# Optimization experiments

Hardware: AMD Instinct MI355X
Metric: run time of the kernel (lower is better)

## Reference

```python
import jax, jax.numpy as jnp
import numpy as np

B, S, D, H, FF, R, NB = 8, 1024, 768, 12, 3072, 16, 768


def _ln(x, g, b, eps=1e-6):
    m = x.mean(-1, keepdims=True)
    v = jnp.mean((x - m) ** 2, axis=-1, keepdims=True)
    return (x - m) * jax.lax.rsqrt(v + eps) * g + b


def setup_inputs() -> dict:
    key = jax.random.key(0)

    def rn(i, shape, s=0.02):
        return jax.random.normal(jax.random.fold_in(key, i), shape, jnp.float32) * s

    inp = {
        "x": jax.random.normal(jax.random.fold_in(key, 0), (B, S, D), jnp.float32),
        "attn_mask": jnp.zeros((S, S), jnp.float32),
        "norm1_g": jnp.ones((D,), jnp.float32),
        "norm1_b": jnp.zeros((D,), jnp.float32),
        "q_w": rn(1, (D, D)), "q_b": jnp.zeros((D,), jnp.float32),
        "k_w": rn(2, (D, D)), "k_b": jnp.zeros((D,), jnp.float32),
        "v_w": rn(3, (D, D)), "v_b": jnp.zeros((D,), jnp.float32),
        "o_w": rn(4, (D, D)), "o_b": jnp.zeros((D,), jnp.float32),
        "norm2_g": jnp.ones((D,), jnp.float32),
        "norm2_b": jnp.zeros((D,), jnp.float32),
        "fc1_w": rn(5, (FF, D)), "fc1_b": jnp.zeros((FF,), jnp.float32),
        "fc2_w": rn(6, (D, FF)), "fc2_b": jnp.zeros((D,), jnp.float32),
        # shared LoRA (backbone tokens)
        "lora1_A": rn(7, (D, R)), "lora1_B": rn(8, (R, FF)),
        "lora2_A": rn(9, (FF, R)), "lora2_B": rn(10, (R, D)),
        # expert VeRA: frozen shared A/B, per-expert diagonal scaling vectors
        "vera1_A": rn(11, (D, R)), "vera1_B": rn(12, (R, FF)),
        "vera2_A": rn(13, (FF, R)), "vera2_B": rn(14, (R, D)),
        "expert_fc1_d": rn(15, (R,), 1.0), "expert_fc1_b": rn(16, (FF,), 1.0),
        "expert_fc2_d": rn(17, (R,), 1.0), "expert_fc2_b": rn(18, (D,), 1.0),
        "num_backbone_tokens": NB,
    }
    return inp


def reference(x, attn_mask, norm1_g, norm1_b, q_w, q_b, k_w, k_b, v_w, v_b,
              o_w, o_b, norm2_g, norm2_b, fc1_w, fc1_b, fc2_w, fc2_b,
              lora1_A, lora1_B, lora2_A, lora2_B,
              vera1_A, vera1_B, vera2_A, vera2_B,
              expert_fc1_d, expert_fc1_b, expert_fc2_d, expert_fc2_b,
              num_backbone_tokens):
    bsz, seq, dim = x.shape
    hd = dim // H                      # head_dim = 64
    scale = hd ** -0.5
    nb = num_backbone_tokens

    # ---- attention (manual bmm + mask + softmax, eval-mode dropout = identity) ----
    h = _ln(x, norm1_g, norm1_b)
    q = (h @ q_w.T + q_b).reshape(bsz, seq, H, hd)
    k = (h @ k_w.T + k_b).reshape(bsz, seq, H, hd)
    v = (h @ v_w.T + v_b).reshape(bsz, seq, H, hd)
    scores = jnp.einsum('bqhd,bkhd->bhqk', q * scale, k) + attn_mask  # [B,H,S,S]
    probs = jax.nn.softmax(scores, axis=-1)
    ao = jnp.einsum('bhqk,bkhd->bqhd', probs, v).reshape(bsz, seq, dim)
    x = x + (ao @ o_w.T + o_b)

    # ---- MLP with split backbone (shared LoRA) / expert (VeRA) adapters ----
    residual = x
    n2 = _ln(x, norm2_g, norm2_b)
    hid = n2 @ fc1_w.T + fc1_b                                   # [B,S,FF]
    hid_b = hid[:, :nb] + (n2[:, :nb] @ lora1_A) @ lora1_B
    hid_e = hid[:, nb:] + (((n2[:, nb:] @ vera1_A) * expert_fc1_d) @ vera1_B) * expert_fc1_b
    hid = jnp.concatenate([hid_b, hid_e], axis=1)
    hid = jax.nn.gelu(hid)
    out = hid @ fc2_w.T + fc2_b                                  # [B,S,D]
    out_b = out[:, :nb] + (hid[:, :nb] @ lora2_A) @ lora2_B
    out_e = out[:, nb:] + (((hid[:, nb:] @ vera2_A) * expert_fc2_d) @ vera2_B) * expert_fc2_b
    out = jnp.concatenate([out_b, out_e], axis=1)
    return residual + out
```

## Files before the change

kernel.cpp:

```cpp
#include <hip/hip_runtime.h>
#include <stdint.h>

#define B_  8
#define S_  1024
#define D_  768
#define H_  12
#define HD_ 64
#define FF_ 3072
#define M_  (B_*S_)
#define R_  16
#define QLD 2304
#define KBLK 128

typedef unsigned short u16;
typedef short s16x8 __attribute__((ext_vector_type(8)));
typedef float fx4  __attribute__((ext_vector_type(4)));

__device__ __forceinline__ float b2f(u16 u) {
  union { unsigned int i; float f; } c; c.i = ((unsigned int)u) << 16; return c.f;
}
__device__ __forceinline__ u16 f2b(float f) {
  union { float f; unsigned int i; } c; c.f = f;
  unsigned int x = c.i;
  x += 0x7FFFu + ((x >> 16) & 1u);
  return (u16)(x >> 16);
}
__device__ __forceinline__ float gelu_f(float x) {
  float u = 0.7978845608028654f * (x + 0.044715f * x * x * x);
  float e = __expf(2.f * u);
  float t = 1.f - 2.f / (e + 1.f);
  return 0.5f * x * (1.f + t);
}
__device__ __forceinline__ void gload16(const u16* gsrc, u16* ldst) {
  __builtin_amdgcn_global_load_lds(
      (__attribute__((address_space(1))) void*)(gsrc),
      (__attribute__((address_space(3))) void*)(ldst), 16, 0, 0);
}

__global__ __launch_bounds__(256)
void cvt_all(const float* __restrict__ q_w, const float* __restrict__ k_w,
             const float* __restrict__ v_w, const float* __restrict__ o_w,
             const float* __restrict__ fc1_w, const float* __restrict__ fc2_w,
             u16* __restrict__ wqkv, u16* __restrict__ wo,
             u16* __restrict__ wfc1, u16* __restrict__ wfc2)
{
  const int i = blockIdx.x * 256 + threadIdx.x;
  const int q1  = D_ * D_ / 4;
  const int fd4 = FF_ * D_ / 4;
  const float* s; u16* d; int j;
  if      (i <     q1)       { s = q_w;   d = wqkv;            j = i; }
  else if (i < 2 * q1)       { s = k_w;   d = wqkv + D_*D_;    j = i - q1; }
  else if (i < 3 * q1)       { s = v_w;   d = wqkv + 2*D_*D_;  j = i - 2*q1; }
  else if (i < 4 * q1)       { s = o_w;   d = wo;              j = i - 3*q1; }
  else if (i < 4 * q1 + fd4) { s = fc1_w; d = wfc1;            j = i - 4*q1; }
  else                       { s = fc2_w; d = wfc2;            j = i - 4*q1 - fd4; }
  const float4 f = ((const float4*)s)[j];
  ushort4 o4; o4.x = f2b(f.x); o4.y = f2b(f.y); o4.z = f2b(f.z); o4.w = f2b(f.w);
  ((ushort4*)d)[j] = o4;
}

__global__ __launch_bounds__(256)
void prep_all(const float* __restrict__ q_bv, const float* __restrict__ k_bv,
              const float* __restrict__ v_bv, float* __restrict__ qkvb,
              const float* __restrict__ lora1B, const float* __restrict__ vera1B,
              const float* __restrict__ e1b, u16* __restrict__ up1L, u16* __restrict__ up1V,
              const float* __restrict__ lora2B, const float* __restrict__ vera2B,
              const float* __restrict__ e2b, u16* __restrict__ up2L, u16* __restrict__ up2V,
              const float* __restrict__ lora2A, const float* __restrict__ vera2A,
              u16* __restrict__ a2tL, u16* __restrict__ a2tV)
{
  const int f = blockIdx.x * 256 + threadIdx.x;
  if (f < QLD)
    qkvb[f] = (f < D_) ? q_bv[f] : (f < 2 * D_) ? k_bv[f - D_] : v_bv[f - 2 * D_];
  {
    const float ev = e1b[f];
    #pragma unroll
    for (int r = 0; r < 16; ++r) {
      up1L[(size_t)f * 32 + r] = f2b(lora1B[(size_t)r * FF_ + f]);
      up1V[(size_t)f * 32 + r] = f2b(vera1B[(size_t)r * FF_ + f] * ev);
      up1L[(size_t)f * 32 + 16 + r] = 0;
      up1V[(size_t)f * 32 + 16 + r] = 0;
    }
  }
  {
    const float4* apl = (const float4*)(lora2A + (size_t)f * 16);
    const float4* apv = (const float4*)(vera2A + (size_t)f * 16);
    #pragma unroll
    for (int q4 = 0; q4 < 4; ++q4) {
      const float4 l4 = apl[q4], v4 = apv[q4];
      a2tL[(size_t)(q4*4+0) * FF_ + f] = f2b(l4.x);
      a2tL[(size_t)(q4*4+1) * FF_ + f] = f2b(l4.y);
      a2tL[(size_t)(q4*4+2) * FF_ + f] = f2b(l4.z);
      a2tL[(size_t)(q4*4+3) * FF_ + f] = f2b(l4.w);
      a2tV[(size_t)(q4*4+0) * FF_ + f] = f2b(v4.x);
      a2tV[(size_t)(q4*4+1) * FF_ + f] = f2b(v4.y);
      a2tV[(size_t)(q4*4+2) * FF_ + f] = f2b(v4.z);
      a2tV[(size_t)(q4*4+3) * FF_ + f] = f2b(v4.w);
    }
  }
  if (f < D_) {
    const float ev = e2b[f];
    #pragma unroll
    for (int r = 0; r < 16; ++r) {
      up2L[(size_t)f * 32 + r] = f2b(lora2B[(size_t)r * D_ + f]);
      up2V[(size_t)f * 32 + r] = f2b(vera2B[(size_t)r * D_ + f] * ev);
      up2L[(size_t)f * 32 + 16 + r] = 0;
      up2V[(size_t)f * 32 + 16 + r] = 0;
    }
  }
}

template<bool ADD>
__global__ __launch_bounds__(256)
void ln_k(const float* __restrict__ x, const u16* __restrict__ add,
          const float* __restrict__ g, const float* __restrict__ beta,
          u16* __restrict__ outb, float* __restrict__ xsum,
          const float* __restrict__ Alora, const float* __restrict__ Avera,
          const float* __restrict__ dvec, u16* __restrict__ tmp1b,
          const int* __restrict__ nbp)
{
  const int row = blockIdx.x;
  const size_t base = (size_t)row * D_;
  float v0[3]; float s = 0.f, sq = 0.f;
  #pragma unroll
  for (int i = 0; i < 3; ++i) {
    const int d = threadIdx.x + i * 256;
    float val = x[base + d];
    if (ADD) { val += b2f(add[base + d]); xsum[base + d] = val; }
    v0[i] = val; s += val; sq += val * val;
  }
  #pragma unroll
  for (int mm = 32; mm >= 1; mm >>= 1) { s += __shfl_xor(s, mm); sq += __shfl_xor(sq, mm); }
  __shared__ float ss[4], s2[4];
  if ((threadIdx.x & 63) == 0) { ss[threadIdx.x >> 6] = s; s2[threadIdx.x >> 6] = sq; }
  __syncthreads();
  s  = ss[0] + ss[1] + ss[2] + ss[3];
  sq = s2[0] + s2[1] + s2[2] + s2[3];
  const float mean = s * (1.f / D_);
  const float var  = sq * (1.f / D_) - mean * mean;
  const float rs   = rsqrtf(var + 1e-6f);
  float nv[3];
  #pragma unroll
  for (int i = 0; i < 3; ++i) {
    const int d = threadIdx.x + i * 256;
    nv[i] = (v0[i] - mean) * rs * g[d] + beta[d];
    outb[base + d] = f2b(nv[i]);
  }

  if (ADD) {
    const int nb = *nbp;
    const bool ex = (row % S_) >= nb;
    const float* Am = ex ? Avera : Alora;
    float p[16];
    #pragma unroll
    for (int r = 0; r < 16; ++r) p[r] = 0.f;
    #pragma unroll
    for (int i = 0; i < 3; ++i) {
      const int d = threadIdx.x + i * 256;
      const float4* ap = (const float4*)(Am + (size_t)d * R_);
      const float4 a0 = ap[0], a1 = ap[1], a2 = ap[2], a3 = ap[3];
      const float vv = nv[i];
      p[0]  += vv * a0.x; p[1]  += vv * a0.y; p[2]  += vv * a0.z; p[3]  += vv * a0.w;
      p[4]  += vv * a1.x; p[5]  += vv * a1.y; p[6]  += vv * a1.z; p[7]  += vv * a1.w;
      p[8]  += vv * a2.x; p[9]  += vv * a2.y; p[10] += vv * a2.z; p[11] += vv * a2.w;
      p[12] += vv * a3.x; p[13] += vv * a3.y; p[14] += vv * a3.z; p[15] += vv * a3.w;
    }
    #pragma unroll
    for (int st = 1; st < 16; st <<= 1)
      #pragma unroll
      for (int r = 0; r < 16; ++r) p[r] += __shfl_xor(p[r], st);
    __shared__ float sred[16][16];
    const int grp = threadIdx.x >> 4;
    if ((threadIdx.x & 15) == 0) {
      #pragma unroll
      for (int r = 0; r < 16; ++r) sred[grp][r] = p[r];
    }
    __syncthreads();
    if (threadIdx.x < 16) {
      float v = 0.f;
      #pragma unroll
      for (int gg = 0; gg < 16; ++gg) v += sred[gg][threadIdx.x];
      if (ex) v *= dvec[threadIdx.x];
      tmp1b[(size_t)row * 32 + threadIdx.x] = f2b(v);
      tmp1b[(size_t)row * 32 + 16 + threadIdx.x] = 0;
    }
  }
}

template<int MODE>
__global__ __launch_bounds__(256)
void gemm_bt(const u16* __restrict__ A, const u16* __restrict__ W,
             const float* __restrict__ bias, u16* __restrict__ Cb,
             float* __restrict__ Cf, const float* __restrict__ resid,
             const u16* __restrict__ Aad, const u16* __restrict__ BadL,
             const u16* __restrict__ BadV, const int* __restrict__ nbp,
             int M, int N, int K)
{
  __shared__ u16 As[128 * 32];
  __shared__ u16 Bs[128 * 32];
  const int tid   = threadIdx.x;
  const int lane  = tid & 63;
  const int wid   = tid >> 6;
  const int wr    = wid >> 1;
  const int wc    = wid & 1;
  const int lr    = lane & 15;
  const int lk    = (lane >> 4) << 3;
  const int gn    = N >> 7;
  const int nwg   = (M >> 7) * gn;
  const int chunk = nwg >> 3;
  const int lin   = blockIdx.x;
  const int swz   = (lin & 7) * chunk + (lin >> 3);
  const int m0    = (swz / gn) * 128;
  const int n0    = (swz % gn) * 128;
  const int kg    = (tid & 3) * 8;
  const int row_a = tid >> 2;

  fx4 acc[4][4];
  const fx4 zero = {0.f, 0.f, 0.f, 0.f};
  #pragma unroll
  for (int i = 0; i < 4; ++i)
    #pragma unroll
    for (int j = 0; j < 4; ++j) acc[i][j] = zero;

  for (int k0 = 0; k0 < K; k0 += 32) {
    #pragma unroll
    for (int u = 0; u < 2; ++u) {
      const int row = u * 64 + row_a;
      const int li  = u * 256 + tid;
      gload16(A + (size_t)(m0 + row) * K + k0 + kg, &As[li * 8]);
      gload16(W + (size_t)(n0 + row) * K + k0 + kg, &Bs[li * 8]);
    }
    __syncthreads();
    s16x8 av[4], bv[4];
    #pragma unroll
    for (int i = 0; i < 4; ++i)
      av[i] = *(const s16x8*)&As[(wr * 64 + i * 16 + lr) * 32 + lk];
    #pragma unroll
    for (int j = 0; j < 4; ++j)
      bv[j] = *(const s16x8*)&Bs[(wc * 64 + j * 16 + lr) * 32 + lk];
    #pragma unroll
    for (int i = 0; i < 4; ++i)
      #pragma unroll
      for (int j = 0; j < 4; ++j)
        acc[i][j] = __builtin_amdgcn_mfma_f32_16x16x32_bf16(av[i], bv[j], acc[i][j], 0, 0, 0);
    __syncthreads();
  }

  if (MODE >= 1) {
    const int nbb = *nbp;
    const u16* Bad = ((m0 % S_) >= nbb) ? BadV : BadL;
    #pragma unroll
    for (int u = 0; u < 2; ++u) {
      const int row = u * 64 + row_a;
      const int li  = u * 256 + tid;
      gload16(Aad + (size_t)(m0 + row) * 32 + kg, &As[li * 8]);
      gload16(Bad + (size_t)(n0 + row) * 32 + kg, &Bs[li * 8]);
    }
    __syncthreads();
    s16x8 av[4], bv[4];
    #pragma unroll
    for (int i = 0; i < 4; ++i)
      av[i] = *(const s16x8*)&As[(wr * 64 + i * 16 + lr) * 32 + lk];
    #pragma unroll
    for (int j = 0; j < 4; ++j)
      bv[j] = *(const s16x8*)&Bs[(wc * 64 + j * 16 + lr) * 32 + lk];
    #pragma unroll
    for (int i = 0; i < 4; ++i)
      #pragma unroll
      for (int j = 0; j < 4; ++j)
        acc[i][j] = __builtin_amdgcn_mfma_f32_16x16x32_bf16(av[i], bv[j], acc[i][j], 0, 0, 0);
    __syncthreads();
  }

  const int rb = (lane >> 4) * 4;
  #pragma unroll
  for (int j = 0; j < 4; ++j) {
    const int col = n0 + wc * 64 + j * 16 + lr;
    const float bj = bias ? bias[col] : 0.f;
    #pragma unroll
    for (int i = 0; i < 4; ++i) {
      const int row = m0 + wr * 64 + i * 16 + rb;
      #pragma unroll
      for (int r = 0; r < 4; ++r) {
        const float val = acc[i][j][r] + bj;
        const size_t idx = (size_t)(row + r) * N + col;
        if (MODE == 1)      Cb[idx] = f2b(gelu_f(val));
        else if (MODE == 2) Cf[idx] = resid[idx] + val;
        else                Cb[idx] = f2b(val);
      }
    }
  }
}

__global__ __launch_bounds__(256)
void downproj(const u16* __restrict__ hid, const u16* __restrict__ A2tL,
              const u16* __restrict__ A2tV, float* __restrict__ part,
              const int* __restrict__ nbp)
{
  __shared__ u16 As[128 * 32];
  __shared__ u16 Bs[16 * 32];
  const int tid  = threadIdx.x;
  const int lane = tid & 63;
  const int w    = tid >> 6;
  const int lr   = lane & 15;
  const int lk   = (lane >> 4) << 3;
  const int m0   = blockIdx.x * 128;
  const int kb   = blockIdx.y * (FF_ / 8);
  const int nb   = *nbp;
  const u16* A2t = ((m0 % S_) >= nb) ? A2tV : A2tL;
  const int kg    = (tid & 3) * 8;
  const int row_a = tid >> 2;

  const fx4 zero = {0.f, 0.f, 0.f, 0.f};
  fx4 acc[2]; acc[0] = zero; acc[1] = zero;

  for (int k0 = kb; k0 < kb + FF_ / 8; k0 += 32) {
    #pragma unroll
    for (int u = 0; u < 2; ++u)
      gload16(hid + (size_t)(m0 + u * 64 + row_a) * FF_ + k0 + kg,
              &As[(u * 256 + tid) * 8]);
    if (tid < 64)
      gload16(A2t + (size_t)(tid >> 2) * FF_ + k0 + kg, &Bs[tid * 8]);
    __syncthreads();
    s16x8 bv = *(const s16x8*)&Bs[lr * 32 + lk];
    #pragma unroll
    for (int i = 0; i < 2; ++i) {
      s16x8 av = *(const s16x8*)&As[(w * 32 + i * 16 + lr) * 32 + lk];
      acc[i] = __builtin_amdgcn_mfma_f32_16x16x32_bf16(av, bv, acc[i], 0, 0, 0);
    }
    __syncthreads();
  }

  const int rb = (lane >> 4) * 4;
  #pragma unroll
  for (int i = 0; i < 2; ++i)
    #pragma unroll
    for (int r = 0; r < 4; ++r)
      part[(size_t)blockIdx.y * M_ * 16 +
           (size_t)(m0 + w * 32 + i * 16 + rb + r) * 16 + lr] = acc[i][r];
}

__global__ __launch_bounds__(256)
void reduce_dp(const float* __restrict__ part, const float* __restrict__ d2,
               u16* __restrict__ tmp2b, const int* __restrict__ nbp)
{
  const int idx = blockIdx.x * 256 + threadIdx.x;
  const int m = idx >> 4, r = idx & 15;
  const int nb = *nbp;
  float s = 0.f;
  #pragma unroll
  for (int ks = 0; ks < 8; ++ks) s += part[(size_t)ks * M_ * 16 + idx];
  if ((m % S_) >= nb) s *= d2[r];
  tmp2b[(size_t)m * 32 + r] = f2b(s);
  tmp2b[(size_t)m * 32 + 16 + r] = 0;
}

__global__ __launch_bounds__(256)
void attn_mfma(const u16* __restrict__ qkv, const float* __restrict__ mask,
               u16* __restrict__ o)
{
  __shared__ u16 Kl[2][128 * 64];
  __shared__ u16 Vt[2][64 * 128];
  __shared__ uint32_t Pl[4][1024];

  const int tid  = threadIdx.x;
  const int lane = tid & 63;
  const int wq   = tid >> 6;
  const int lr   = lane & 15;
  const int hi   = lane >> 4;
  const int lin = blockIdx.x;
  const int vsw = (lin & 7) * 192 + (lin >> 3);
  const int qb  = vsw & 15;
  const int bh  = vsw >> 4;
  const int b    = bh / H_;
  const int h    = bh % H_;
  const size_t tok0 = (size_t)b * S_ + (size_t)qb * 64;
  const size_t colh = (size_t)h * HD_;

  const int va  = tid >> 3;
  const int vc8 = (tid & 7) * 8;
  u16* qstage = (u16*)&Pl[0][0];

  #pragma unroll
  for (int u = 0; u < 2; ++u) {
    const int li = u * 256 + tid;
    const int r  = li >> 3;
    const int cb = ((li & 7) ^ (r & 7)) * 8;
    gload16(qkv + (tok0 + r) * QLD + colh + cb, &qstage[li * 8]);
  }
  {
    const size_t ktok = (size_t)b * S_;
    #pragma unroll
    for (int u = 0; u < 4; ++u) {
      const int li = u * 256 + tid;
      const int r  = li >> 3;
      const int cb = ((li & 7) ^ (r & 7)) * 8;
      gload16(qkv + (ktok + r) * QLD + D_ + colh + cb, &Kl[0][li * 8]);
    }
    const u16* vp = qkv + (ktok + 4 * va) * QLD + 2 * D_ + colh + vc8;
    s16x8 w0 = *(const s16x8*)vp;
    s16x8 w1 = *(const s16x8*)(vp + QLD);
    s16x8 w2 = *(const s16x8*)(vp + 2 * QLD);
    s16x8 w3 = *(const s16x8*)(vp + 3 * QLD);
    #pragma unroll
    for (int jj = 0; jj < 8; ++jj) {
      const int d  = vc8 + jj;
      const int sw = ((d & 7) ^ ((d >> 3) & 7)) << 3;
      const int cp = (4 * va) ^ sw;
      *(uint32_t*)&Vt[0][d * 128 + cp] =
          (uint32_t)(u16)w0[jj] | ((uint32_t)(u16)w1[jj] << 16);
      *(uint32_t*)&Vt[0][d * 128 + cp + 2] =
          (uint32_t)(u16)w2[jj] | ((uint32_t)(u16)w3[jj] << 16);
    }
  }
  __syncthreads();

  s16x8 qa[2];
  {
    const int qrow = wq * 16 + lr;
    #pragma unroll
    for (int ks = 0; ks < 2; ++ks)
      qa[ks] = *(const s16x8*)&qstage[qrow * 64 + ((ks * 32 + hi * 8) ^ ((qrow & 7) << 3))];
  }
  __syncthreads();

  const fx4 zero = {0.f, 0.f, 0.f, 0.f};
  fx4 oacc[4];
  #pragma unroll
  for (int dj = 0; dj < 4; ++dj) oacc[dj] = zero;
  float mreg = -3.0e38f, lreg = 0.f;

  const int NT = S_ / KBLK;
  for (int kt = 0; kt < NT; ++kt) {
    const int cur = kt & 1;
    const int nxt = cur ^ 1;

    s16x8 w0, w1, w2, w3;
    if (kt + 1 < NT) {
      const size_t ktokn = (size_t)b * S_ + (size_t)(kt + 1) * KBLK;
      #pragma unroll
      for (int u = 0; u < 4; ++u) {
        const int li = u * 256 + tid;
        const int r  = li >> 3;
        const int cb = ((li & 7) ^ (r & 7)) * 8;
        gload16(qkv + (ktokn + r) * QLD + D_ + colh + cb, &Kl[nxt][li * 8]);
      }
      const u16* vp = qkv + (ktokn + 4 * va) * QLD + 2 * D_ + colh + vc8;
      w0 = *(const s16x8*)vp;
      w1 = *(const s16x8*)(vp + QLD);
      w2 = *(const s16x8*)(vp + 2 * QLD);
      w3 = *(const s16x8*)(vp + 3 * QLD);
    }

    float val[8][4];
    #pragma unroll
    for (int jh = 0; jh < 2; ++jh) {
      s16x8 kb2[4][2];
      #pragma unroll
      for (int j = 0; j < 4; ++j) {
        const int n = (jh * 4 + j) * 16 + lr;
        #pragma unroll
        for (int ks = 0; ks < 2; ++ks)
          kb2[j][ks] = *(const s16x8*)&Kl[cur][n * 64 + ((ks * 32 + hi * 8) ^ ((n & 7) << 3))];
      }
      fx4 m4[4];
      {
        const float* mp = mask + (size_t)(qb * 64 + wq * 16 + lr) * S_
                        + (size_t)kt * KBLK + jh * 64 + 4 * hi;
        #pragma unroll
        for (int j = 0; j < 4; ++j)
          m4[j] = *(const fx4*)(mp + j * 16);
      }
      fx4 sf[4];
      #pragma unroll
      for (int j = 0; j < 4; ++j) sf[j] = zero;
      __builtin_amdgcn_s_setprio(1);
      #pragma unroll
      for (int ks = 0; ks < 2; ++ks)
        #pragma unroll
        for (int j = 0; j < 4; ++j)
          sf[j] = __builtin_amdgcn_mfma_f32_16x16x32_bf16(kb2[j][ks], qa[ks], sf[j], 0, 0, 0);
      __builtin_amdgcn_s_setprio(0);
      #pragma unroll
      for (int j = 0; j < 4; ++j)
        #pragma unroll
        for (int r = 0; r < 4; ++r)
          val[jh * 4 + j][r] = sf[j][r] * 0.125f + m4[j][r];
    }

    {
      float mk[8];
      #pragma unroll
      for (int kg = 0; kg < 8; ++kg)
        mk[kg] = fmaxf(fmaxf(val[kg][0], val[kg][1]), fmaxf(val[kg][2], val[kg][3]));
      float mx = fmaxf(fmaxf(fmaxf(mk[0], mk[1]), fmaxf(mk[2], mk[3])),
                       fmaxf(fmaxf(mk[4], mk[5]), fmaxf(mk[6], mk[7])));
      mx = fmaxf(mx, __shfl_xor(mx, 16));
      mx = fmaxf(mx, __shfl_xor(mx, 32));
      const float mn  = fmaxf(mreg, mx);
      const float fac = __expf(mreg - mn);
      mreg = mn;
      float sk[8];
      #pragma unroll
      for (int kg = 0; kg < 8; ++kg) {
        #pragma unroll
        for (int r = 0; r < 4; ++r) val[kg][r] = __expf(val[kg][r] - mn);
        sk[kg] = (val[kg][0] + val[kg][1]) + (val[kg][2] + val[kg][3]);
      }
      float rs = ((sk[0] + sk[1]) + (sk[2] + sk[3])) + ((sk[4] + sk[5]) + (sk[6] + sk[7]));
      rs += __shfl_xor(rs, 16);
      rs += __shfl_xor(rs, 32);
      lreg = lreg * fac + rs;
      float facr[4];
      #pragma unroll
      for (int r = 0; r < 4; ++r) facr[r] = __shfl(fac, hi * 4 + r);
      #pragma unroll
      for (int dj = 0; dj < 4; ++dj)
        #pragma unroll
        for (int r = 0; r < 4; ++r) oacc[dj][r] *= facr[r];
    }

    {
      uint32_t* prow = &Pl[wq][lr * 64];
      #pragma unroll
      for (int kg = 0; kg < 8; ++kg) {
        const uint32_t p0 = __builtin_amdgcn_perm(
            __float_as_uint(val[kg][1]), __float_as_uint(val[kg][0]), 0x07060302u);
        const uint32_t p1 = __builtin_amdgcn_perm(
            __float_as_uint(val[kg][3]), __float_as_uint(val[kg][2]), 0x07060302u);
        const int i0 = (8 * kg + 2 * hi) ^ ((lr & 7) << 3);
        uint2 pk; pk.x = p0; pk.y = p1;
        *(uint2*)&prow[i0] = pk;
      }
    }

    if (kt + 1 < NT) {
      #pragma unroll
      for (int jj = 0; jj < 8; ++jj) {
        const int d  = vc8 + jj;
        const int sw = ((d & 7) ^ ((d >> 3) & 7)) << 3;
        const int cp = (4 * va) ^ sw;
        *(uint32_t*)&Vt[nxt][d * 128 + cp] =
            (uint32_t)(u16)w0[jj] | ((uint32_t)(u16)w1[jj] << 16);
        *(uint32_t*)&Vt[nxt][d * 128 + cp + 2] =
            (uint32_t)(u16)w2[jj] | ((uint32_t)(u16)w3[jj] << 16);
      }
    }

    #pragma unroll
    for (int ks = 0; ks < 4; ++ks) {
      const int pbase = (16 * ks + 4 * hi) ^ ((lr & 7) << 3);
      s16x8 pa = *(const s16x8*)&Pl[wq][lr * 64 + pbase];
      s16x8 bv2[4];
      #pragma unroll
      for (int dj = 0; dj < 4; ++dj) {
        const int n  = dj * 16 + lr;
        const int sw = ((n & 7) ^ ((n >> 3) & 7)) << 3;
        bv2[dj] = *(const s16x8*)&Vt[cur][n * 128 + ((ks * 32 + hi * 8) ^ sw)];
      }
      __builtin_amdgcn_s_setprio(1);
      #pragma unroll
      for (int dj = 0; dj < 4; ++dj)
        oacc[dj] = __builtin_amdgcn_mfma_f32_16x16x32_bf16(pa, bv2[dj], oacc[dj], 0, 0, 0);
      __builtin_amdgcn_s_setprio(0);
    }

    __syncthreads();
  }

  {
    const float linv = 1.f / lreg;
    float invr[4];
    #pragma unroll
    for (int r = 0; r < 4; ++r) invr[r] = __shfl(linv, hi * 4 + r);
    #pragma unroll
    for (int r = 0; r < 4; ++r) {
      const size_t grow = (tok0 + wq * 16 + hi * 4 + r) * D_ + colh;
      #pragma unroll
      for (int dj = 0; dj < 4; ++dj)
        o[grow + dj * 16 + lr] = f2b(oacc[dj][r] * invr[r]);
    }
  }
}

extern "C" void kernel_launch(void* const* d_in, const int* in_sizes, int n_in,
                              void* d_out, int out_size, void* d_ws, size_t ws_size,
                              hipStream_t stream)
{
  const float* x      = (const float*)d_in[0];
  const float* mask   = (const float*)d_in[1];
  const float* n1g    = (const float*)d_in[2];
  const float* n1b    = (const float*)d_in[3];
  const float* q_w    = (const float*)d_in[4];
  const float* q_bv   = (const float*)d_in[5];
  const float* k_w    = (const float*)d_in[6];
  const float* k_bv   = (const float*)d_in[7];
  const float* v_w    = (const float*)d_in[8];
  const float* v_bv   = (const float*)d_in[9];
  const float* o_w    = (const float*)d_in[10];
  const float* o_bv   = (const float*)d_in[11];
  const float* n2g    = (const float*)d_in[12];
  const float* n2b    = (const float*)d_in[13];
  const float* fc1_w  = (const float*)d_in[14];
  const float* fc1_bv = (const float*)d_in[15];
  const float* fc2_w  = (const float*)d_in[16];
  const float* fc2_bv = (const float*)d_in[17];
  const float* lora1A = (const float*)d_in[18];
  const float* lora1B = (const float*)d_in[19];
  const float* lora2A = (const float*)d_in[20];
  const float* lora2B = (const float*)d_in[21];
  const float* vera1A = (const float*)d_in[22];
  const float* vera1B = (const float*)d_in[23];
  const float* vera2A = (const float*)d_in[24];
  const float* vera2B = (const float*)d_in[25];
  const float* e1d    = (const float*)d_in[26];
  const float* e1b    = (const float*)d_in[27];
  const float* e2d    = (const float*)d_in[28];
  const float* e2b    = (const float*)d_in[29];
  const int*   nbp    = (const int*)d_in[30];

  char* wsb = (char*)d_ws;
  u16* h1    = (u16*)wsb; wsb += (size_t)M_ * D_ * 2;
  u16* qkv   = (u16*)wsb; wsb += (size_t)M_ * QLD * 2;
  u16* attno = (u16*)wsb; wsb += (size_t)M_ * D_ * 2;
  u16* oproj = (u16*)wsb; wsb += (size_t)M_ * D_ * 2;
  u16* n2    = (u16*)wsb; wsb += (size_t)M_ * D_ * 2;
  u16* wqkv  = (u16*)wsb; wsb += (size_t)QLD * D_ * 2;
  u16* wo    = (u16*)wsb; wsb += (size_t)D_ * D_ * 2;
  u16* wfc1  = (u16*)wsb; wsb += (size_t)FF_ * D_ * 2;
  u16* wfc2  = (u16*)wsb; wsb += (size_t)D_ * FF_ * 2;
  u16* tmp1b = (u16*)wsb; wsb += (size_t)M_ * 32 * 2;
  u16* tmp2b = (u16*)wsb; wsb += (size_t)M_ * 32 * 2;
  u16* up1L  = (u16*)wsb; wsb += (size_t)FF_ * 32 * 2;
  u16* up1V  = (u16*)wsb; wsb += (size_t)FF_ * 32 * 2;
  u16* up2L  = (u16*)wsb; wsb += (size_t)D_ * 32 * 2;
  u16* up2V  = (u16*)wsb; wsb += (size_t)D_ * 32 * 2;
  u16* a2tL  = (u16*)wsb; wsb += (size_t)16 * FF_ * 2;
  u16* a2tV  = (u16*)wsb; wsb += (size_t)16 * FF_ * 2;
  float* qkvb = (float*)wsb; wsb += (size_t)QLD * 4;
  float* part = (float*)wsb; wsb += (size_t)8 * M_ * 16 * 4;
  u16* hidb = h1;

  const int totq = (4 * D_ * D_ + 2 * FF_ * D_) / 4;
  cvt_all<<<totq / 256, 256, 0, stream>>>(q_w, k_w, v_w, o_w, fc1_w, fc2_w,
                                          wqkv, wo, wfc1, wfc2);
  prep_all<<<FF_ / 256, 256, 0, stream>>>(q_bv, k_bv, v_bv, qkvb,
                                          lora1B, vera1B, e1b, up1L, up1V,
                                          lora2B, vera2B, e2b, up2L, up2V,
                                          lora2A, vera2A, a2tL, a2tV);

  ln_k<false><<<M_, 256, 0, stream>>>(x, nullptr, n1g, n1b, h1, nullptr,
                                      nullptr, nullptr, nullptr, nullptr, nullptr);
  gemm_bt<0><<<(M_/128) * (QLD/128), 256, 0, stream>>>(
      h1, wqkv, qkvb, qkv, nullptr, nullptr, nullptr, nullptr, nullptr, nullptr,
      M_, QLD, D_);
  attn_mfma<<<(S_/64) * (B_*H_), 256, 0, stream>>>(qkv, mask, attno);
  gemm_bt<0><<<(M_/128) * (D_/128), 256, 0, stream>>>(
      attno, wo, o_bv, oproj, nullptr, nullptr, nullptr, nullptr, nullptr, nullptr,
      M_, D_, D_);

  ln_k<true><<<M_, 256, 0, stream>>>(x, oproj, n2g, n2b, n2, (float*)d_out,
                                     lora1A, vera1A, e1d, tmp1b, nbp);

  gemm_bt<1><<<(M_/128) * (FF_/128), 256, 0, stream>>>(
      n2, wfc1, fc1_bv, hidb, nullptr, nullptr, tmp1b, up1L, up1V, nbp,
      M_, FF_, D_);

  downproj<<<dim3(M_/128, 8), 256, 0, stream>>>(hidb, a2tL, a2tV, part, nbp);
  reduce_dp<<<M_*16/256, 256, 0, stream>>>(part, e2d, tmp2b, nbp);

  gemm_bt<2><<<(M_/128) * (D_/128), 256, 0, stream>>>(
      hidb, wfc2, fc2_bv, nullptr, (float*)d_out, (const float*)d_out,
      tmp2b, up2L, up2V, nbp, M_, D_, FF_);
}
```

Measured before the change: 380.7 us.

## Double-buffer LDS tiles in GEMM and downproj kernels to overlap loads

The main bf16 GEMM and the LoRA/VeRA down-projection kernel now ping-pong between two shared-memory buffers. The next K-slice is prefetched while MFMAs run on the current one, which removes one barrier per iteration. The adapter rank-32 tail is folded in as an extra pipeline stage. Wave priority is raised around the MFMA block. LDS use doubles, which may lower occupancy, and correctness depends on whether gload16 is a synchronous or direct-to-LDS load.

```diff
diff --git a/kernel.cpp b/kernel.cpp
--- a/kernel.cpp
+++ b/kernel.cpp
@@ -196,8 +196,8 @@
              const u16* __restrict__ BadV, const int* __restrict__ nbp,
              int M, int N, int K)
 {
-  __shared__ u16 As[128 * 32];
-  __shared__ u16 Bs[128 * 32];
+  __shared__ u16 As[2][128 * 32];
+  __shared__ u16 Bs[2][128 * 32];
   const int tid   = threadIdx.x;
   const int lane  = tid & 63;
   const int wid   = tid >> 6;
@@ -215,6 +215,15 @@
   const int kg    = (tid & 3) * 8;
   const int row_a = tid >> 2;
 
+  const int nst = K >> 5;
+  const int tot = (MODE >= 1) ? nst + 1 : nst;
+  const u16* Bad = nullptr;
+  if (MODE >= 1) Bad = ((m0 % S_) >= *nbp) ? BadV : BadL;
+
+  const u16* arow = A + (size_t)(m0 + row_a) * K + kg;
+  const u16* wrow = W + (size_t)(n0 + row_a) * K + kg;
+  const size_t half_a = (size_t)64 * K;
+
   fx4 acc[4][4];
   const fx4 zero = {0.f, 0.f, 0.f, 0.f};
   #pragma unroll
@@ -222,53 +231,43 @@
     #pragma unroll
     for (int j = 0; j < 4; ++j) acc[i][j] = zero;
 
-  for (int k0 = 0; k0 < K; k0 += 32) {
-    #pragma unroll
-    for (int u = 0; u < 2; ++u) {
-      const int row = u * 64 + row_a;
-      const int li  = u * 256 + tid;
-      gload16(A + (size_t)(m0 + row) * K + k0 + kg, &As[li * 8]);
-      gload16(W + (size_t)(n0 + row) * K + k0 + kg, &Bs[li * 8]);
-    }
-    __syncthreads();
+  gload16(arow,          &As[0][tid * 8]);
+  gload16(arow + half_a, &As[0][(256 + tid) * 8]);
+  gload16(wrow,          &Bs[0][tid * 8]);
+  gload16(wrow + half_a, &Bs[0][(256 + tid) * 8]);
+  __syncthreads();
+
+  for (int t = 0; t < tot; ++t) {
+    const int cur = t & 1;
+    if (t + 1 < tot) {
+      const int nxt = cur ^ 1;
+      if (MODE >= 1 && t + 1 == nst) {
+        gload16(Aad + (size_t)(m0 + row_a) * 32 + kg,      &As[nxt][tid * 8]);
+        gload16(Aad + (size_t)(m0 + 64 + row_a) * 32 + kg, &As[nxt][(256 + tid) * 8]);
+        gload16(Bad + (size_t)(n0 + row_a) * 32 + kg,      &Bs[nxt][tid * 8]);
+        gload16(Bad + (size_t)(n0 + 64 + row_a) * 32 + kg, &Bs[nxt][(256 + tid) * 8]);
+      } else {
+        const size_t ko = (size_t)(t + 1) * 32;
+        gload16(arow + ko,          &As[nxt][tid * 8]);
+        gload16(arow + ko + half_a, &As[nxt][(256 + tid) * 8]);
+        gload16(wrow + ko,          &Bs[nxt][tid * 8]);
+        gload16(wrow + ko + half_a, &Bs[nxt][(256 + tid) * 8]);
+      }
+    }
     s16x8 av[4], bv[4];
     #pragma unroll
     for (int i = 0; i < 4; ++i)
-      av[i] = *(const s16x8*)&As[(wr * 64 + i * 16 + lr) * 32 + lk];
+      av[i] = *(const s16x8*)&As[cur][(wr * 64 + i * 16 + lr) * 32 + lk];
     #pragma unroll
     for (int j = 0; j < 4; ++j)
-      bv[j] = *(const s16x8*)&Bs[(wc * 64 + j * 16 + lr) * 32 + lk];
+      bv[j] = *(const s16x8*)&Bs[cur][(wc * 64 + j * 16 + lr) * 32 + lk];
+    __builtin_amdgcn_s_setprio(1);
     #pragma unroll
     for (int i = 0; i < 4; ++i)
       #pragma unroll
       for (int j = 0; j < 4; ++j)
         acc[i][j] = __builtin_amdgcn_mfma_f32_16x16x32_bf16(av[i], bv[j], acc[i][j], 0, 0, 0);
-    __syncthreads();
-  }
-
-  if (MODE >= 1) {
-    const int nbb = *nbp;
-    const u16* Bad = ((m0 % S_) >= nbb) ? BadV : BadL;
-    #pragma unroll
-    for (int u = 0; u < 2; ++u) {
-      const int row = u * 64 + row_a;
-      const int li  = u * 256 + tid;
-      gload16(Aad + (size_t)(m0 + row) * 32 + kg, &As[li * 8]);
-      gload16(Bad + (size_t)(n0 + row) * 32 + kg, &Bs[li * 8]);
-    }
-    __syncthreads();
-    s16x8 av[4], bv[4];
-    #pragma unroll
-    for (int i = 0; i < 4; ++i)
-      av[i] = *(const s16x8*)&As[(wr * 64 + i * 16 + lr) * 32 + lk];
-    #pragma unroll
-    for (int j = 0; j < 4; ++j)
-      bv[j] = *(const s16x8*)&Bs[(wc * 64 + j * 16 + lr) * 32 + lk];
-    #pragma unroll
-    for (int i = 0; i < 4; ++i)
-      #pragma unroll
-      for (int j = 0; j < 4; ++j)
-        acc[i][j] = __builtin_amdgcn_mfma_f32_16x16x32_bf16(av[i], bv[j], acc[i][j], 0, 0, 0);
+    __builtin_amdgcn_s_setprio(0);
     __syncthreads();
   }
 
@@ -297,8 +296,8 @@
               const u16* __restrict__ A2tV, float* __restrict__ part,
               const int* __restrict__ nbp)
 {
-  __shared__ u16 As[128 * 32];
-  __shared__ u16 Bs[16 * 32];
+  __shared__ u16 As[2][128 * 32];
+  __shared__ u16 Bs[2][16 * 32];
   const int tid  = threadIdx.x;
   const int lane = tid & 63;
   const int w    = tid >> 6;
@@ -311,21 +310,32 @@
   const int kg    = (tid & 3) * 8;
   const int row_a = tid >> 2;
 
+  const u16* hrow = hid + (size_t)(m0 + row_a) * FF_ + kb + kg;
+  const size_t half_h = (size_t)64 * FF_;
+  const u16* brow = A2t + (size_t)(tid >> 2) * FF_ + kb + kg;
+
   const fx4 zero = {0.f, 0.f, 0.f, 0.f};
   fx4 acc[2]; acc[0] = zero; acc[1] = zero;
 
-  for (int k0 = kb; k0 < kb + FF_ / 8; k0 += 32) {
-    #pragma unroll
-    for (int u = 0; u < 2; ++u)
-      gload16(hid + (size_t)(m0 + u * 64 + row_a) * FF_ + k0 + kg,
-              &As[(u * 256 + tid) * 8]);
-    if (tid < 64)
-      gload16(A2t + (size_t)(tid >> 2) * FF_ + k0 + kg, &Bs[tid * 8]);
-    __syncthreads();
-    s16x8 bv = *(const s16x8*)&Bs[lr * 32 + lk];
+  const int nst = (FF_ / 8) >> 5;
+  gload16(hrow,          &As[0][tid * 8]);
+  gload16(hrow + half_h, &As[0][(256 + tid) * 8]);
+  if (tid < 64) gload16(brow, &Bs[0][tid * 8]);
+  __syncthreads();
+
+  for (int t = 0; t < nst; ++t) {
+    const int cur = t & 1;
+    if (t + 1 < nst) {
+      const int nxt = cur ^ 1;
+      const size_t ko = (size_t)(t + 1) * 32;
+      gload16(hrow + ko,          &As[nxt][tid * 8]);
+      gload16(hrow + ko + half_h, &As[nxt][(256 + tid) * 8]);
+      if (tid < 64) gload16(brow + ko, &Bs[nxt][tid * 8]);
+    }
+    s16x8 bv = *(const s16x8*)&Bs[cur][lr * 32 + lk];
     #pragma unroll
     for (int i = 0; i < 2; ++i) {
-      s16x8 av = *(const s16x8*)&As[(w * 32 + i * 16 + lr) * 32 + lk];
+      s16x8 av = *(const s16x8*)&As[cur][(w * 32 + i * 16 + lr) * 32 + lk];
       acc[i] = __builtin_amdgcn_mfma_f32_16x16x32_bf16(av, bv, acc[i], 0, 0, 0);
     }
     __syncthreads();
```

After: 369.4 us. 1.03x faster.
